# Kernel tuning notes

Hardware: AMD Instinct MI355X
Metric: run time of the kernel (lower is better)

Reference implementation:

```python
import jax, jax.numpy as jnp
import numpy as np
from functools import partial

LEAK = 1.0 / 3.0   # scn default leakiness 0.333
EPS = 1e-4         # scn BatchNormalization default eps


def linkey(c, S):
    return (c[..., 0] * S + c[..., 1]) * S + c[..., 2]


def sub_offsets(K):
    r = K // 2
    g = np.stack(np.meshgrid(*([np.arange(-r, r + 1)] * 3), indexing='ij'), -1).reshape(-1, 3)
    return jnp.asarray(g, jnp.int32)


def down_offsets(s):
    g = np.stack(np.meshgrid(*([np.arange(s)] * 3), indexing='ij'), -1).reshape(-1, 3)
    return jnp.asarray(g, jnp.int32)


@partial(jax.checkpoint, static_argnums=(4, 5))
def sparse_conv(out_coords, in_coords, in_feats, W, S_in, stride, offsets):
    """Rulebook gather-GEMM-scatter via sorted-key binary search.
    out_coords [M,3], in_coords [N,3] sorted by linearized key, in_feats [N,Cin],
    W [K3,Cin,Cout]. Submanifold: stride=1, centered offsets, out_coords==in_coords.
    Strided scn.Convolution: offsets 0..stride-1, out sites = unique(in//stride)."""
    in_keys = linkey(in_coords, S_in)  # sorted [N]
    Nin = in_keys.shape[0]

    def body(acc, kw):
        off, Wk = kw
        child = out_coords * stride + off                       # [M,3]
        valid = jnp.all((child >= 0) & (child < S_in), axis=-1)
        nkey = linkey(child, S_in)
        idx = jnp.searchsorted(in_keys, nkey)
        idxc = jnp.clip(idx, 0, Nin - 1)
        found = valid & (in_keys[idxc] == nkey)
        g = jnp.where(found[:, None], in_feats[idxc], 0.0)      # gather, zero for inactive
        return acc + g @ Wk, None

    acc0 = jnp.zeros((out_coords.shape[0], W.shape[-1]), in_feats.dtype)
    acc, _ = jax.lax.scan(body, acc0, (offsets, W))
    return acc


def bn_lrelu(x, g, b):
    m = x.mean(0)
    v = x.var(0)
    y = (x - m) * (g / jnp.sqrt(v + EPS)) + b
    return jnp.where(y > 0, y, LEAK * y)


def lrelu(x):
    return jnp.where(x > 0, x, LEAK * x)


def forward_core(floats, c0, c1, c2, c3, c4):
    (feats0, W_init, Wd1, gd1, bd1, W11a, g11, b11, W11b,
     W12a, g12, b12, W12b, Wd2, gd2, bd2,
     W21a, g21, b21, W21b, W22a, g22, b22, W22b,
     Wd3, gd3, bd3, Wd4, gd4, bd4, W2, b2, W3, b3) = floats
    o3 = sub_offsets(3)
    x = sparse_conv(c0, c0, feats0, W_init, 512, 1, sub_offsets(7))                 # [N0,64] @512
    x = bn_lrelu(sparse_conv(c1, c0, x, Wd1, 512, 2, down_offsets(2)), gd1, bd1)    # [N1,64] @256
    res = x
    h = bn_lrelu(sparse_conv(c1, c1, x, W11a, 256, 1, o3), g11, b11)
    x = lrelu(sparse_conv(c1, c1, h, W11b, 256, 1, o3) + res)
    res = x
    h = bn_lrelu(sparse_conv(c1, c1, x, W12a, 256, 1, o3), g12, b12)
    x = lrelu(sparse_conv(c1, c1, h, W12b, 256, 1, o3) + res)
    x = bn_lrelu(sparse_conv(c2, c1, x, Wd2, 256, 2, down_offsets(2)), gd2, bd2)    # [N2,128] @128
    res = x
    h = bn_lrelu(sparse_conv(c2, c2, x, W21a, 128, 1, o3), g21, b21)
    x = lrelu(sparse_conv(c2, c2, h, W21b, 128, 1, o3) + res)
    res = x
    h = bn_lrelu(sparse_conv(c2, c2, x, W22a, 128, 1, o3), g22, b22)
    x = lrelu(sparse_conv(c2, c2, h, W22b, 128, 1, o3) + res)
    x = bn_lrelu(sparse_conv(c3, c2, x, Wd3, 128, 4, down_offsets(4)), gd3, bd3)    # [N3,64] @32
    x = bn_lrelu(sparse_conv(c4, c3, x, Wd4, 32, 4, down_offsets(4)), gd4, bd4)     # [N4,2]  @8
    # SparseToDense -> dense [2,8,8,8], then torch .view(-1, 2*8*8*8) (channel-major)
    k4 = linkey(c4, 8)
    dense = jnp.zeros((8 * 8 * 8, 2), x.dtype).at[k4].set(x)    # [512,2]
    flat = dense.T.reshape(1, -1)                               # [1,1024]
    v = jax.nn.elu(flat @ W2 + b2)
    return jax.nn.sigmoid(v @ W3 + b3)                          # [1,1]


def _decode(k, S):
    a = k // (S * S)
    r = k % (S * S)
    return np.stack([a, r // S, r % S], -1).astype(np.int32)


def setup_inputs() -> dict:
    rng = np.random.default_rng(0)
    N0 = 50000
    k0 = np.unique(rng.integers(0, 512 ** 3, size=N0 + 20000))[:N0]
    c0 = _decode(k0, 512)
    c1 = _decode(np.unique((c0[:, 0].astype(np.int64) // 2 * 256 + c0[:, 1] // 2) * 256 + c0[:, 2] // 2), 256)
    c2 = _decode(np.unique((c1[:, 0].astype(np.int64) // 2 * 128 + c1[:, 1] // 2) * 128 + c1[:, 2] // 2), 128)
    c3 = _decode(np.unique((c2[:, 0].astype(np.int64) // 4 * 32 + c2[:, 1] // 4) * 32 + c2[:, 2] // 4), 32)
    c4 = _decode(np.unique((c3[:, 0].astype(np.int64) // 4 * 8 + c3[:, 1] // 4) * 8 + c3[:, 2] // 4), 8)
    key = jax.random.key(0)
    ks = jax.random.split(key, 20)

    def w(i, shape, fan):
        return jax.random.normal(ks[i], shape, jnp.float32) / np.float32(np.sqrt(fan))

    return dict(
        feats0=jax.random.normal(ks[0], (N0, 1), jnp.float32),
        W_init=w(1, (343, 1, 64), 343.0),
        Wd1=w(2, (8, 64, 64), 8 * 64), gd1=jnp.ones(64), bd1=jnp.zeros(64),
        W11a=w(3, (27, 64, 64), 27 * 64), g11=jnp.ones(64), b11=jnp.zeros(64),
        W11b=w(4, (27, 64, 64), 27 * 64),
        W12a=w(5, (27, 64, 64), 27 * 64), g12=jnp.ones(64), b12=jnp.zeros(64),
        W12b=w(6, (27, 64, 64), 27 * 64),
        Wd2=w(7, (8, 64, 128), 8 * 64), gd2=jnp.ones(128), bd2=jnp.zeros(128),
        W21a=w(8, (27, 128, 128), 27 * 128), g21=jnp.ones(128), b21=jnp.zeros(128),
        W21b=w(9, (27, 128, 128), 27 * 128),
        W22a=w(10, (27, 128, 128), 27 * 128), g22=jnp.ones(128), b22=jnp.zeros(128),
        W22b=w(11, (27, 128, 128), 27 * 128),
        Wd3=w(12, (64, 128, 64), 64 * 128), gd3=jnp.ones(64), bd3=jnp.zeros(64),
        Wd4=w(13, (64, 64, 2), 64 * 64), gd4=jnp.ones(2), bd4=jnp.zeros(2),
        W2=w(14, (1024, 2), 1024.0), b2=jnp.zeros(2),
        W3=w(15, (2, 1), 2.0), b3=jnp.zeros(1),
        coords0=jnp.asarray(c0), coords1=jnp.asarray(c1), coords2=jnp.asarray(c2),
        coords3=jnp.asarray(c3), coords4=jnp.asarray(c4),
    )


def reference(feats0, W_init, Wd1, gd1, bd1, W11a, g11, b11, W11b, W12a, g12, b12, W12b,
              Wd2, gd2, bd2, W21a, g21, b21, W21b, W22a, g22, b22, W22b,
              Wd3, gd3, bd3, Wd4, gd4, bd4, W2, b2, W3, b3,
              coords0, coords1, coords2, coords3, coords4):
    floats = (feats0, W_init, Wd1, gd1, bd1, W11a, g11, b11, W11b, W12a, g12, b12, W12b,
              Wd2, gd2, bd2, W21a, g21, b21, W21b, W22a, g22, b22, W22b,
              Wd3, gd3, bd3, Wd4, gd4, bd4, W2, b2, W3, b3)
    return forward_core(floats, coords0, coords1, coords2, coords3, coords4)
```

## Files before the change

### kernel.cpp

```cpp
#include <hip/hip_runtime.h>

#define LEAKF (1.0f/3.0f)
#define BN_EPS 1e-4f

__device__ __forceinline__ unsigned hmix(int key) {
    unsigned h = (unsigned)key * 2654435761u;
    h ^= h >> 15;
    return h;
}

__device__ __forceinline__ int hlookup(const int* __restrict__ hk,
                                       const int* __restrict__ hv,
                                       int mask, int key) {
    unsigned h = hmix(key) & (unsigned)mask;
    while (true) {
        int k = hk[h];
        if (k == key) return hv[h];
        if (k == -1) return -1;
        h = (h + 1) & (unsigned)mask;
    }
}

__device__ __forceinline__ float bnl(float v, float s, float h) {
    v = v * s + h;
    return v > 0.f ? v : v * LEAKF;
}

__global__ __launch_bounds__(256) void build_hash_bm_all(
    int B0, int B1, int B2,
    int N0, const int* __restrict__ c0, int* __restrict__ hk0, int* __restrict__ hv0,
    int m0, unsigned* __restrict__ bm0,
    int N1, const int* __restrict__ c1, int* __restrict__ hk1, int* __restrict__ hv1,
    int m1, unsigned* __restrict__ bm1,
    int N2, const int* __restrict__ c2, int* __restrict__ hk2, int* __restrict__ hv2,
    int m2, unsigned* __restrict__ bm2,
    int N3, const int* __restrict__ c3, int* __restrict__ hk3, int* __restrict__ hv3,
    int m3) {
    const int* coords; int* hk; int* hv; unsigned* bm; int mask, S, N, i;
    int b = blockIdx.x;
    if (b < B0)           { coords = c0; hk = hk0; hv = hv0; bm = bm0; mask = m0; S = 512; N = N0; i = b * 256 + threadIdx.x; }
    else if (b < B0 + B1) { coords = c1; hk = hk1; hv = hv1; bm = bm1; mask = m1; S = 256; N = N1; i = (b - B0) * 256 + threadIdx.x; }
    else if (b < B0 + B1 + B2) { coords = c2; hk = hk2; hv = hv2; bm = bm2; mask = m2; S = 128; N = N2; i = (b - B0 - B1) * 256 + threadIdx.x; }
    else                  { coords = c3; hk = hk3; hv = hv3; bm = nullptr; mask = m3; S = 32; N = N3; i = (b - B0 - B1 - B2) * 256 + threadIdx.x; }
    if (i >= N) return;
    int key = (coords[3 * i] * S + coords[3 * i + 1]) * S + coords[3 * i + 2];
    if (bm) atomicOr(&bm[key >> 5], 1u << (key & 31));
    unsigned h = hmix(key) & (unsigned)mask;
    while (true) {
        int old = atomicCAS(&hk[h], -1, key);
        if (old == -1 || old == key) { hv[h] = i; break; }
        h = (h + 1) & (unsigned)mask;
    }
}

__global__ __launch_bounds__(256) void rb_sub_bm(
    int B1,
    int N1, const int* __restrict__ c1, const unsigned* __restrict__ bm1,
    const int* __restrict__ hk1, const int* __restrict__ hv1, int m1,
    int2* __restrict__ rb1, int* __restrict__ cnt1, int cap1,
    int N2, const int* __restrict__ c2, const unsigned* __restrict__ bm2,
    const int* __restrict__ hk2, const int* __restrict__ hv2, int m2,
    int2* __restrict__ rb2, int* __restrict__ cnt2, int cap2) {
    __shared__ int lcnt[27];
    __shared__ int lbase[27];
    int tid = threadIdx.x;
    if (tid < 27) lcnt[tid] = 0;
    __syncthreads();
    const int* coords; const unsigned* bm; const int* hk; const int* hv;
    int mask, S, N, t; int2* pairs; int* counts; int cap;
    if (blockIdx.x < B1) {
        coords = c1; bm = bm1; hk = hk1; hv = hv1; mask = m1; S = 256; N = N1;
        pairs = rb1; counts = cnt1; cap = cap1; t = blockIdx.x * 256 + tid;
    } else {
        coords = c2; bm = bm2; hk = hk2; hv = hv2; mask = m2; S = 128; N = N2;
        pairs = rb2; counts = cnt2; cap = cap2; t = (blockIdx.x - B1) * 256 + tid;
    }
    unsigned bits = 0;
    int m = 0, kmin = 0, z = 0, dx = 0, dy = 0;
    int rk[3], ix[3];
    if (t < N * 9) {
        m = t / 9;
        int od = t - m * 9;
        dx = od / 3 - 1;
        dy = od - (od / 3) * 3 - 1;
        int x = coords[3 * m] + dx;
        int y = coords[3 * m + 1] + dy;
        z = coords[3 * m + 2];
        if ((unsigned)x < (unsigned)S && (unsigned)y < (unsigned)S) {
            int zmin = z - 1 < 0 ? 0 : z - 1;
            int zmax = z + 1 > S - 1 ? S - 1 : z + 1;
            kmin = (x * S + y) * S + zmin;
            int wi = kmin >> 5, sh = kmin & 31, nb = zmax - zmin + 1;
            unsigned long long w =
                ((unsigned long long)bm[wi + 1] << 32) | (unsigned long long)bm[wi];
            bits = (unsigned)((w >> sh) & ((1u << nb) - 1u));
            if (dx == 0 && dy == 0) bits &= ~(1u << (z - zmin));
            unsigned tmp = bits;
            int nf = 0;
            while (tmp) {
                int bb = __ffs(tmp) - 1;
                tmp &= tmp - 1;
                ix[nf] = hlookup(hk, hv, mask, kmin + bb);
                int dz = (kmin & (S - 1)) + bb - z;
                int k = (dx + 1) * 9 + (dy + 1) * 3 + (dz + 1);
                rk[nf] = atomicAdd(&lcnt[k], 1);
                nf++;
            }
        }
    }
    __syncthreads();
    if (tid < 27 && lcnt[tid] > 0) lbase[tid] = atomicAdd(&counts[tid], lcnt[tid]);
    __syncthreads();
    {
        unsigned tmp = bits;
        int j = 0;
        while (tmp) {
            int bb = __ffs(tmp) - 1;
            tmp &= tmp - 1;
            int dz = (kmin & (S - 1)) + bb - z;
            int k = (dx + 1) * 9 + (dy + 1) * 3 + (dz + 1);
            int p = lbase[k] + rk[j];
            if (p < cap) pairs[(size_t)k * cap + p] = make_int2(m, ix[j]);
            j++;
        }
    }
}

__global__ __launch_bounds__(256) void rb_down_all(
    int B1, int B2,
    int N0, const int* __restrict__ c0, const int* __restrict__ hk1,
    const int* __restrict__ hv1, int m1, int2* __restrict__ rbD1,
    int* __restrict__ cntD1, int capD1,
    int N1, const int* __restrict__ c1, const int* __restrict__ hk2,
    const int* __restrict__ hv2, int m2, int2* __restrict__ rbD2,
    int* __restrict__ cntD2, int capD2,
    int N2, const int* __restrict__ c2, const int* __restrict__ hk3,
    const int* __restrict__ hv3, int m3, int2* __restrict__ rbD3,
    int* __restrict__ cntD3, int capD3) {
    __shared__ int lcnt[64];
    __shared__ int lbase[64];
    int tid = threadIdx.x;
    const int* cin; const int* hk; const int* hv;
    int mask, Sout, s, Nin, i; int2* pairs; int* counts; int cap;
    int b = blockIdx.x;
    if (b < B1) {
        cin = c0; hk = hk1; hv = hv1; mask = m1; Sout = 256; s = 2; Nin = N0;
        pairs = rbD1; counts = cntD1; cap = capD1; i = b * 256 + tid;
    } else if (b < B1 + B2) {
        cin = c1; hk = hk2; hv = hv2; mask = m2; Sout = 128; s = 2; Nin = N1;
        pairs = rbD2; counts = cntD2; cap = capD2; i = (b - B1) * 256 + tid;
    } else {
        cin = c2; hk = hk3; hv = hv3; mask = m3; Sout = 32; s = 4; Nin = N2;
        pairs = rbD3; counts = cntD3; cap = capD3; i = (b - B1 - B2) * 256 + tid;
    }
    int K3 = s * s * s;
    if (tid < K3) lcnt[tid] = 0;
    __syncthreads();
    int k = -1, m = -1, rank = 0;
    if (i < Nin) {
        int x = cin[3 * i], y = cin[3 * i + 1], z = cin[3 * i + 2];
        k = ((x % s) * s + (y % s)) * s + (z % s);
        int key = ((x / s) * Sout + (y / s)) * Sout + (z / s);
        m = hlookup(hk, hv, mask, key);
        rank = atomicAdd(&lcnt[k], 1);
    }
    __syncthreads();
    if (tid < K3 && lcnt[tid] > 0) lbase[tid] = atomicAdd(&counts[tid], lcnt[tid]);
    __syncthreads();
    if (i < Nin) {
        int p = lbase[k] + rank;
        if (p < cap) pairs[(size_t)k * cap + p] = make_int2(m, i);
    }
}

__global__ __launch_bounds__(256) void init_probe(
    int total, int chunk, const int* __restrict__ c0, const unsigned* __restrict__ bm,
    const int* __restrict__ hk, const int* __restrict__ hv, int mask,
    int2* __restrict__ pairs, int* __restrict__ pcount, int cap) {
    __shared__ int lcnt, lbase;
    int tid = threadIdx.x;
    if (tid == 0) lcnt = 0;
    __syncthreads();
    int b = blockIdx.x;
    int nb = (b & 7) * chunk + (b >> 3);
    int t = nb * 256 + tid;
    unsigned bitsArr[7];
    int kminArr[7];
#pragma unroll
    for (int j = 0; j < 7; j++) { bitsArr[j] = 0; kminArr[j] = 0; }
    int m = -1, z = 0, dx = 0, rank = 0, found = 0;
    if (t < total) {
        m = t / 7;
        dx = t - m * 7 - 3;
        int x = c0[3 * m] + dx;
        int cy = c0[3 * m + 1];
        z = c0[3 * m + 2];
        if ((unsigned)x < 512u) {
            int zmin = z - 3 < 0 ? 0 : z - 3;
            int zmax = z + 3 > 511 ? 511 : z + 3;
            int nbits = zmax - zmin + 1;
#pragma unroll
            for (int j = 0; j < 7; j++) {
                int y = cy + j - 3;
                if ((unsigned)y < 512u) {
                    int kmin = (x * 512 + y) * 512 + zmin;
                    kminArr[j] = kmin;
                    int wi = kmin >> 5, sh = kmin & 31;
                    unsigned long long w =
                        ((unsigned long long)bm[wi + 1] << 32) | (unsigned long long)bm[wi];
                    unsigned bits = (unsigned)((w >> sh) & ((1u << nbits) - 1u));
                    if (dx == 0 && j == 3) bits &= ~(1u << (z - zmin));
                    bitsArr[j] = bits;
                    found += __popc(bits);
                }
            }
        }
    }
    if (found) rank = atomicAdd(&lcnt, found);
    __syncthreads();
    if (tid == 0 && lcnt > 0) lbase = atomicAdd(pcount, lcnt);
    __syncthreads();
    if (found) {
        int p = lbase + rank;
#pragma unroll
        for (int j = 0; j < 7; j++) {
            unsigned bits = bitsArr[j];
            while (bits) {
                int b2 = __ffs(bits) - 1;
                bits &= bits - 1;
                int nkey = kminArr[j] + b2;
                int idx = hlookup(hk, hv, mask, nkey);
                int dz = (kminArr[j] & 511) + b2 - z;
                int k = (dx + 3) * 49 + j * 7 + (dz + 3);
                if (p < cap) pairs[p] = make_int2(m, idx | (k << 17));
                p++;
            }
        }
    }
}

__global__ __launch_bounds__(256) void init_center(
    int N0, const float* __restrict__ f0, const float* __restrict__ W,
    float* __restrict__ out) {
    int t = blockIdx.x * 256 + threadIdx.x;
    if (t >= N0 * 64) return;
    int m = t >> 6, co = t & 63;
    out[t] = f0[m] * W[171 * 64 + co];
}

__global__ __launch_bounds__(256) void init_apply(
    const int2* __restrict__ pairs, const int* __restrict__ pcount, int cap,
    const float* __restrict__ f0, const float* __restrict__ W,
    float* __restrict__ out) {
    int P = min(*pcount, cap);
    int t = blockIdx.x * 256 + threadIdx.x;
    if (t >= P * 64) return;
    int p = t >> 6, co = t & 63;
    int2 pr = pairs[p];
    int idx = pr.y & 0x1FFFF, k = pr.y >> 17;
    atomicAdd(&out[(size_t)pr.x * 64 + co], f0[idx] * W[k * 64 + co]);
}

template <int C, int TS, bool BNF>
__global__ __launch_bounds__(256) void center_gemm(
    int N, const float* __restrict__ inF, const float* __restrict__ Wc,
    float* __restrict__ out, const float* __restrict__ scp,
    const float* __restrict__ shp) {
    constexpr int C4 = C / 4;
    constexpr int SP = TS / 8;
    __shared__ float sW[C * 64];
    __shared__ float4 sRow[TS * C4];
    int tid = threadIdx.x;
    int t0 = blockIdx.x * TS;
    int co0 = blockIdx.y << 6;
    for (int e = tid; e < C * 16; e += 256) {
        int ci = e >> 4, c4 = e & 15;
        ((float4*)sW)[e] = *(const float4*)(Wc + (size_t)ci * C + co0 + c4 * 4);
    }
    for (int e = tid; e < TS * C4; e += 256) {
        int p = e / C4, c4 = e - p * C4;
        float4 v = make_float4(0.f, 0.f, 0.f, 0.f);
        if (t0 + p < N) {
            v = ((const float4*)inF)[(size_t)(t0 + p) * C4 + c4];
            if (BNF) {
                float4 s4 = ((const float4*)scp)[c4];
                float4 h4 = ((const float4*)shp)[c4];
                v.x = bnl(v.x, s4.x, h4.x);
                v.y = bnl(v.y, s4.y, h4.y);
                v.z = bnl(v.z, s4.z, h4.z);
                v.w = bnl(v.w, s4.w, h4.w);
            }
        }
        sRow[e] = v;
    }
    __syncthreads();
    int co = tid & 31, sg = tid >> 5;
    float accA[SP], accB[SP];
#pragma unroll
    for (int j = 0; j < SP; j++) { accA[j] = 0.f; accB[j] = 0.f; }
    for (int c4 = 0; c4 < C4; c4++) {
        float a0 = sW[(c4 * 4 + 0) * 64 + co];
        float a1 = sW[(c4 * 4 + 1) * 64 + co];
        float a2 = sW[(c4 * 4 + 2) * 64 + co];
        float a3 = sW[(c4 * 4 + 3) * 64 + co];
        float b0 = sW[(c4 * 4 + 0) * 64 + co + 32];
        float b1 = sW[(c4 * 4 + 1) * 64 + co + 32];
        float b2 = sW[(c4 * 4 + 2) * 64 + co + 32];
        float b3 = sW[(c4 * 4 + 3) * 64 + co + 32];
#pragma unroll
        for (int j = 0; j < SP; j++) {
            float4 r = sRow[(sg * SP + j) * C4 + c4];
            accA[j] += r.x * a0 + r.y * a1 + r.z * a2 + r.w * a3;
            accB[j] += r.x * b0 + r.y * b1 + r.z * b2 + r.w * b3;
        }
    }
#pragma unroll
    for (int j = 0; j < SP; j++) {
        int p = sg * SP + j;
        if (t0 + p < N) {
            out[(size_t)(t0 + p) * C + co0 + co] = accA[j];
            out[(size_t)(t0 + p) * C + co0 + co + 32] = accB[j];
        }
    }
}

template <int CIN, int P, int MODE>
__global__ __launch_bounds__(256) void pair_gemm(
    const float* __restrict__ inF, const float* __restrict__ inF2,
    const float* __restrict__ W, float* __restrict__ out,
    const int2* __restrict__ pairs, const int* __restrict__ counts,
    int cap, int chunksPerK, int totalNb, int COUT, int nslab,
    const float* __restrict__ scp, const float* __restrict__ shp) {
    constexpr int C4 = CIN / 4;
    constexpr int SP = P / 8;
    __shared__ float sW[CIN * 64];
    __shared__ float4 sRow[P * C4];
    __shared__ int sM[P];
    __shared__ int sIdx[P];
    int b = blockIdx.x;
    int nb = (b & 7) * (gridDim.x >> 3) + (b >> 3);
    if (nb >= totalNb) return;
    int k = nb / chunksPerK;
    int chunk = nb - k * chunksPerK;
    int cnt = min(counts[k], cap);
    int base = chunk * P;
    if (base >= cnt) return;
    int Pact = min(P, cnt - base);
    int tid = threadIdx.x;
    if (tid < P) {
        if (tid < Pact) {
            int2 pr = pairs[(size_t)k * cap + base + tid];
            sM[tid] = pr.x;
            sIdx[tid] = pr.y;
        } else {
            sM[tid] = -1;
            sIdx[tid] = 0;
        }
    }
    __syncthreads();
    int co = tid & 31, sg = tid >> 5;
    for (int s = 0; s < nslab; s++) {
        int co0 = s << 6;
        if (s > 0) __syncthreads();
        const float* gW = W + (size_t)k * CIN * COUT + co0;
        for (int e = tid; e < CIN * 16; e += 256) {
            int ci = e >> 4, c4 = e & 15;
            ((float4*)sW)[e] = *(const float4*)(gW + (size_t)ci * COUT + c4 * 4);
        }
        if (s == 0) {
            for (int e = tid; e < P * C4; e += 256) {
                int p = e / C4, c4 = e - p * C4;
                float4 v = make_float4(0.f, 0.f, 0.f, 0.f);
                if (p < Pact) {
                    v = ((const float4*)inF)[(size_t)sIdx[p] * C4 + c4];
                    if (MODE == 1) {
                        float4 s4 = ((const float4*)scp)[c4];
                        float4 h4 = ((const float4*)shp)[c4];
                        v.x = bnl(v.x, s4.x, h4.x);
                        v.y = bnl(v.y, s4.y, h4.y);
                        v.z = bnl(v.z, s4.z, h4.z);
                        v.w = bnl(v.w, s4.w, h4.w);
                    } else if (MODE == 2) {
                        float4 u = ((const float4*)inF2)[(size_t)sIdx[p] * C4 + c4];
                        v.x += u.x; v.y += u.y; v.z += u.z; v.w += u.w;
                        v.x = v.x > 0.f ? v.x : v.x * LEAKF;
                        v.y = v.y > 0.f ? v.y : v.y * LEAKF;
                        v.z = v.z > 0.f ? v.z : v.z * LEAKF;
                        v.w = v.w > 0.f ? v.w : v.w * LEAKF;
                    }
                }
                sRow[e] = v;
            }
        }
        __syncthreads();
        float accA[SP], accB[SP];
#pragma unroll
        for (int j = 0; j < SP; j++) { accA[j] = 0.f; accB[j] = 0.f; }
        for (int c4 = 0; c4 < C4; c4++) {
            float a0 = sW[(c4 * 4 + 0) * 64 + co];
            float a1 = sW[(c4 * 4 + 1) * 64 + co];
            float a2 = sW[(c4 * 4 + 2) * 64 + co];
            float a3 = sW[(c4 * 4 + 3) * 64 + co];
            float b0 = sW[(c4 * 4 + 0) * 64 + co + 32];
            float b1 = sW[(c4 * 4 + 1) * 64 + co + 32];
            float b2 = sW[(c4 * 4 + 2) * 64 + co + 32];
            float b3 = sW[(c4 * 4 + 3) * 64 + co + 32];
#pragma unroll
            for (int j = 0; j < SP; j++) {
                float4 r = sRow[(sg * SP + j) * C4 + c4];
                accA[j] += r.x * a0 + r.y * a1 + r.z * a2 + r.w * a3;
                accB[j] += r.x * b0 + r.y * b1 + r.z * b2 + r.w * b3;
            }
        }
#pragma unroll
        for (int j = 0; j < SP; j++) {
            int p = sg * SP + j;
            if (p < Pact) {
                atomicAdd(&out[(size_t)sM[p] * COUT + co0 + co], accA[j]);
                atomicAdd(&out[(size_t)sM[p] * COUT + co0 + co + 32], accB[j]);
            }
        }
    }
}

__global__ __launch_bounds__(256) void bn_reduce_fin(
    const float4* __restrict__ X4, int total4, int B4, int C, int Cmask, float invN,
    const float* __restrict__ g, const float* __restrict__ b,
    float* __restrict__ sums, int* __restrict__ done,
    float* __restrict__ sc, float* __restrict__ sh) {
    __shared__ float sS[128];
    __shared__ float sQ[128];
    __shared__ int isLast;
    int tid = threadIdx.x;
    if (tid < C) { sS[tid] = 0.f; sQ[tid] = 0.f; }
    __syncthreads();
    int base4 = blockIdx.x * B4;
    int end4 = min(base4 + B4, total4);
    float s0 = 0.f, s1 = 0.f, s2 = 0.f, s3 = 0.f;
    float q0 = 0.f, q1 = 0.f, q2 = 0.f, q3 = 0.f;
    for (int e4 = base4 + tid; e4 < end4; e4 += 256) {
        float4 v = X4[e4];
        s0 += v.x; q0 += v.x * v.x;
        s1 += v.y; q1 += v.y * v.y;
        s2 += v.z; q2 += v.z * v.z;
        s3 += v.w; q3 += v.w * v.w;
    }
    int c0 = (4 * (base4 + tid)) & Cmask;
    atomicAdd(&sS[c0], s0);               atomicAdd(&sQ[c0], q0);
    atomicAdd(&sS[(c0 + 1) & Cmask], s1); atomicAdd(&sQ[(c0 + 1) & Cmask], q1);
    atomicAdd(&sS[(c0 + 2) & Cmask], s2); atomicAdd(&sQ[(c0 + 2) & Cmask], q2);
    atomicAdd(&sS[(c0 + 3) & Cmask], s3); atomicAdd(&sQ[(c0 + 3) & Cmask], q3);
    __syncthreads();
    if (tid < C) {
        atomicAdd(&sums[tid], sS[tid]);
        atomicAdd(&sums[128 + tid], sQ[tid]);
    }
    __syncthreads();
    if (tid == 0) {
        __threadfence();
        int t = atomicAdd(done, 1);
        isLast = (t == (int)gridDim.x - 1);
    }
    __syncthreads();
    if (isLast) {
        if (tid < C) {
            float v1 = atomicAdd(&sums[tid], 0.0f);
            float v2 = atomicAdd(&sums[128 + tid], 0.0f);
            float mean = v1 * invN;
            float var = v2 * invN - mean * mean;
            float s = g[tid] / sqrtf(var + BN_EPS);
            sc[tid] = s;
            sh[tid] = b[tid] - mean * s;
            sums[tid] = 0.f;
            sums[128 + tid] = 0.f;
        }
        if (tid == 0) *done = 0;
    }
}

__global__ __launch_bounds__(256) void add_lrelu_bn(const float4* __restrict__ A,
                                                    const float4* __restrict__ X,
                                                    float4* __restrict__ Y, int total4,
                                                    int C4mask,
                                                    const float* __restrict__ scp,
                                                    const float* __restrict__ shp) {
    int e = blockIdx.x * 256 + threadIdx.x;
    if (e >= total4) return;
    int c4 = e & C4mask;
    float4 s4 = ((const float4*)scp)[c4];
    float4 h4 = ((const float4*)shp)[c4];
    float4 a = A[e], x = X[e], v;
    v.x = a.x + bnl(x.x, s4.x, h4.x);
    v.y = a.y + bnl(x.y, s4.y, h4.y);
    v.z = a.z + bnl(x.z, s4.z, h4.z);
    v.w = a.w + bnl(x.w, s4.w, h4.w);
    v.x = v.x > 0.f ? v.x : v.x * LEAKF;
    v.y = v.y > 0.f ? v.y : v.y * LEAKF;
    v.z = v.z > 0.f ? v.z : v.z * LEAKF;
    v.w = v.w > 0.f ? v.w : v.w * LEAKF;
    Y[e] = v;
}

__global__ __launch_bounds__(64) void tail_kernel(
    int M, const int* __restrict__ oc, const float* __restrict__ x3,
    const float* __restrict__ W, float* __restrict__ x4,
    const int* __restrict__ hk, const int* __restrict__ hv, int mask,
    const float* __restrict__ scp, const float* __restrict__ shp,
    const float* __restrict__ g4, const float* __restrict__ b4,
    const float* __restrict__ W2, const float* __restrict__ b2,
    const float* __restrict__ W3, const float* __restrict__ b3,
    int* __restrict__ ticket, float* __restrict__ out) {
    __shared__ int sIdx[64];
    __shared__ int sK[64];
    __shared__ int sCount;
    __shared__ int isLast;
    __shared__ float sDense[1024];
    __shared__ float sS[2], sQ[2], ssc[2], ssh[2];
    int m = blockIdx.x, tid = threadIdx.x;
    int cx = oc[3 * m], cy = oc[3 * m + 1], cz = oc[3 * m + 2];
    if (tid == 0) sCount = 0;
    __syncthreads();
    {
        int k = tid;
        int a = k >> 4, b = (k >> 2) & 3, c = k & 3;
        int x = cx * 4 + a, y = cy * 4 + b, z = cz * 4 + c;
        int key = (x * 32 + y) * 32 + z;
        int idx = hlookup(hk, hv, mask, key);
        if (idx >= 0) { int p = atomicAdd(&sCount, 1); sIdx[p] = idx; sK[p] = k; }
    }
    __syncthreads();
    int cnt = sCount;
    float s = scp[tid], h = shp[tid];
    float a0 = 0.f, a1 = 0.f;
    for (int j = 0; j < cnt; j++) {
        int idx = sIdx[j], k = sK[j];
        float f = bnl(x3[(size_t)idx * 64 + tid], s, h);
        const float* wk = W + ((size_t)k * 64 + tid) * 2;
        a0 += f * wk[0];
        a1 += f * wk[1];
    }
    for (int o = 32; o > 0; o >>= 1) {
        a0 += __shfl_down(a0, o);
        a1 += __shfl_down(a1, o);
    }
    if (tid == 0) { x4[2 * m] = a0; x4[2 * m + 1] = a1; }
    __threadfence();
    if (tid == 0) {
        int t = atomicAdd(ticket, 1);
        isLast = (t == (int)gridDim.x - 1);
    }
    __syncthreads();
    if (!isLast) return;
    if (tid < 2) { sS[tid] = 0.f; sQ[tid] = 0.f; }
    for (int i = tid; i < 1024; i += 64) sDense[i] = 0.f;
    __syncthreads();
    float ls = 0.f, lq = 0.f;
    for (int i = tid; i < 2 * M; i += 64) {
        float v = atomicAdd(&x4[i], 0.0f);
        ls += v; lq += v * v;
    }
    atomicAdd(&sS[tid & 1], ls);
    atomicAdd(&sQ[tid & 1], lq);
    __syncthreads();
    if (tid < 2) {
        float mean = sS[tid] / (float)M;
        float var = sQ[tid] / (float)M - mean * mean;
        float sc = g4[tid] / sqrtf(var + BN_EPS);
        ssc[tid] = sc;
        ssh[tid] = b4[tid] - mean * sc;
    }
    __syncthreads();
    for (int i = tid; i < 2 * M; i += 64) {
        int mm = i >> 1, co = i & 1;
        float v = atomicAdd(&x4[i], 0.0f) * ssc[co] + ssh[co];
        v = v > 0.f ? v : v * LEAKF;
        int key = (oc[3 * mm] * 8 + oc[3 * mm + 1]) * 8 + oc[3 * mm + 2];
        sDense[key * 2 + co] = v;
    }
    __syncthreads();
    float h0 = 0.f, h1 = 0.f;
    for (int j = tid; j < 1024; j += 64) {
        int co = j >> 9, k = j & 511;
        float f = sDense[k * 2 + co];
        h0 += f * W2[2 * j];
        h1 += f * W2[2 * j + 1];
    }
    for (int o = 32; o > 0; o >>= 1) {
        h0 += __shfl_down(h0, o);
        h1 += __shfl_down(h1, o);
    }
    if (tid == 0) {
        float v0 = h0 + b2[0];
        float v1 = h1 + b2[1];
        v0 = v0 > 0.f ? v0 : expm1f(v0);
        v1 = v1 > 0.f ? v1 : expm1f(v1);
        float z = v0 * W3[0] + v1 * W3[1] + b3[0];
        out[0] = 1.f / (1.f + expf(-z));
    }
}

extern "C" void kernel_launch(void* const* d_in, const int* in_sizes, int n_in,
                              void* d_out, int out_size, void* d_ws, size_t ws_size,
                              hipStream_t stream) {
    const float* F0    = (const float*)d_in[0];
    const float* Winit = (const float*)d_in[1];
    const float* Wd1   = (const float*)d_in[2];
    const float* gd1   = (const float*)d_in[3];
    const float* bd1   = (const float*)d_in[4];
    const float* W11a  = (const float*)d_in[5];
    const float* g11   = (const float*)d_in[6];
    const float* b11   = (const float*)d_in[7];
    const float* W11b  = (const float*)d_in[8];
    const float* W12a  = (const float*)d_in[9];
    const float* g12   = (const float*)d_in[10];
    const float* b12   = (const float*)d_in[11];
    const float* W12b  = (const float*)d_in[12];
    const float* Wd2   = (const float*)d_in[13];
    const float* gd2   = (const float*)d_in[14];
    const float* bd2   = (const float*)d_in[15];
    const float* W21a  = (const float*)d_in[16];
    const float* g21   = (const float*)d_in[17];
    const float* b21   = (const float*)d_in[18];
    const float* W21b  = (const float*)d_in[19];
    const float* W22a  = (const float*)d_in[20];
    const float* g22   = (const float*)d_in[21];
    const float* b22   = (const float*)d_in[22];
    const float* W22b  = (const float*)d_in[23];
    const float* Wd3   = (const float*)d_in[24];
    const float* gd3   = (const float*)d_in[25];
    const float* bd3   = (const float*)d_in[26];
    const float* Wd4   = (const float*)d_in[27];
    const float* gd4   = (const float*)d_in[28];
    const float* bd4   = (const float*)d_in[29];
    const float* W2    = (const float*)d_in[30];
    const float* b2    = (const float*)d_in[31];
    const float* W3    = (const float*)d_in[32];
    const float* b3    = (const float*)d_in[33];
    const int* c0 = (const int*)d_in[34];
    const int* c1 = (const int*)d_in[35];
    const int* c2 = (const int*)d_in[36];
    const int* c3 = (const int*)d_in[37];
    const int* c4 = (const int*)d_in[38];
    int N0 = in_sizes[34] / 3, N1 = in_sizes[35] / 3, N2 = in_sizes[36] / 3;
    int N3 = in_sizes[37] / 3, N4 = in_sizes[38] / 3;

    char* base = (char*)d_ws;
    size_t off = 0;
    auto alloc = [&](size_t bytes) -> void* {
        void* p = base + off;
        off = (off + bytes + 255) & ~(size_t)255;
        return p;
    };
    const int CAP0 = 262144, CAP = 131072, CAP3 = 65536;
    size_t hs_off = off;
    int* hk0 = (int*)alloc((size_t)CAP0 * 4);
    int* hv0 = (int*)alloc((size_t)CAP0 * 4);
    int* hk1 = (int*)alloc((size_t)CAP * 4);
    int* hv1 = (int*)alloc((size_t)CAP * 4);
    int* hk2 = (int*)alloc((size_t)CAP * 4);
    int* hv2 = (int*)alloc((size_t)CAP * 4);
    int* hk3 = (int*)alloc((size_t)CAP3 * 4);
    int* hv3 = (int*)alloc((size_t)CAP3 * 4);
    size_t he_off = off;
    size_t zs_off = off;
    float* sums = (float*)alloc(256 * 4);
    float* scb = (float*)alloc(8 * 128 * 4);
    float* shb = (float*)alloc(8 * 128 * 4);
    float* x4 = (float*)alloc(1032 * 4);
    int* counts = (int*)alloc(136 * 4);
    unsigned* bm1 = (unsigned*)alloc((size_t)(524288 + 2) * 4);
    unsigned* bm2 = (unsigned*)alloc((size_t)(65536 + 2) * 4);
    size_t ze_off = off;
    int* cntS1 = counts, *cntS2 = counts + 27, *cntD1 = counts + 54, *cntD2 = counts + 62,
       * cntD3 = counts + 70;
    int* done = counts + 134;
    int* pcount = counts + 135;
    const int CAP_S1 = 1024, CAP_S2 = 4096, CAP_D1 = 8192, CAP_D2 = 8192, CAP_D3 = 1024;
    const int CAPP = 16384;
    int2* pairs0 = (int2*)alloc((size_t)CAPP * 8);
    int2* rbS1 = (int2*)alloc((size_t)27 * CAP_S1 * 8);
    int2* rbS2 = (int2*)alloc((size_t)27 * CAP_S2 * 8);
    int2* rbD1 = (int2*)alloc((size_t)8 * CAP_D1 * 8);
    int2* rbD2 = (int2*)alloc((size_t)8 * CAP_D2 * 8);
    int2* rbD3 = (int2*)alloc((size_t)64 * CAP_D3 * 8);
    size_t relems = (size_t)N0 * 64;
    if ((size_t)N2 * 128 > relems) relems = (size_t)N2 * 128;
    float* R1 = (float*)alloc(relems * 4);
    float* R2 = (float*)alloc(relems * 4);
    float* R3 = (float*)alloc(relems * 4);
    unsigned* bm0 = (unsigned*)R1;

    hipMemsetAsync(base + hs_off, 0xFF, he_off - hs_off, stream);
    hipMemsetAsync(base + zs_off, 0x00, ze_off - zs_off, stream);
    hipMemsetAsync(bm0, 0x00, (size_t)(1 << 24) + 64, stream);

    int Bh0 = (N0 + 255) / 256, Bh1 = (N1 + 255) / 256, Bh2 = (N2 + 255) / 256,
        Bh3 = (N3 + 255) / 256;
    build_hash_bm_all<<<Bh0 + Bh1 + Bh2 + Bh3, 256, 0, stream>>>(
        Bh0, Bh1, Bh2,
        N0, c0, hk0, hv0, CAP0 - 1, bm0,
        N1, c1, hk1, hv1, CAP - 1, bm1,
        N2, c2, hk2, hv2, CAP - 1, bm2,
        N3, c3, hk3, hv3, CAP3 - 1);
    int Bs1 = (N1 * 9 + 255) / 256, Bs2 = (N2 * 9 + 255) / 256;
    rb_sub_bm<<<Bs1 + Bs2, 256, 0, stream>>>(
        Bs1,
        N1, c1, bm1, hk1, hv1, CAP - 1, rbS1, cntS1, CAP_S1,
        N2, c2, bm2, hk2, hv2, CAP - 1, rbS2, cntS2, CAP_S2);
    rb_down_all<<<Bh0 + Bh1 + Bh2, 256, 0, stream>>>(
        Bh0, Bh1,
        N0, c0, hk1, hv1, CAP - 1, rbD1, cntD1, CAP_D1,
        N1, c1, hk2, hv2, CAP - 1, rbD2, cntD2, CAP_D2,
        N2, c2, hk3, hv3, CAP3 - 1, rbD3, cntD3, CAP_D3);

    auto bnstats = [&](const float* X, int N, int C, const float* g, const float* b,
                       int slot) {
        int total4 = (N * C + 3) >> 2;
        int B4 = 32 * C;
        int grid = (total4 + B4 - 1) / B4;
        bn_reduce_fin<<<grid, 256, 0, stream>>>((const float4*)X, total4, B4, C, C - 1,
                                                1.0f / (float)N, g, b, sums, done,
                                                scb + slot * 128, shb + slot * 128);
    };
    const int CH_S1 = CAP_S1 / 64;
    const int CH_S2 = CAP_S2 / 32;
    const int CH_D12 = CAP_D1 / 64;
    const int CH_D3 = CAP_D3 / 32;
    auto sub64 = [&](const float* X, const float* W, float* Y, int slot) {
        if (slot >= 0) {
            center_gemm<64, 64, true><<<dim3((N1 + 63) / 64, 1), 256, 0, stream>>>(
                N1, X, W + 13 * 64 * 64, Y, scb + slot * 128, shb + slot * 128);
            pair_gemm<64, 64, 1><<<27 * CH_S1, 256, 0, stream>>>(
                X, nullptr, W, Y, rbS1, cntS1, CAP_S1, CH_S1, 27 * CH_S1, 64, 1,
                scb + slot * 128, shb + slot * 128);
        } else {
            center_gemm<64, 64, false><<<dim3((N1 + 63) / 64, 1), 256, 0, stream>>>(
                N1, X, W + 13 * 64 * 64, Y, nullptr, nullptr);
            pair_gemm<64, 64, 0><<<27 * CH_S1, 256, 0, stream>>>(
                X, nullptr, W, Y, rbS1, cntS1, CAP_S1, CH_S1, 27 * CH_S1, 64, 1,
                nullptr, nullptr);
        }
    };
    auto sub128 = [&](const float* X, const float* W, float* Y, int slot) {
        if (slot >= 0) {
            center_gemm<128, 48, true><<<dim3((N2 + 47) / 48, 2), 256, 0, stream>>>(
                N2, X, W + 13 * 128 * 128, Y, scb + slot * 128, shb + slot * 128);
            pair_gemm<128, 32, 1><<<27 * CH_S2, 256, 0, stream>>>(
                X, nullptr, W, Y, rbS2, cntS2, CAP_S2, CH_S2, 27 * CH_S2, 128, 2,
                scb + slot * 128, shb + slot * 128);
        } else {
            center_gemm<128, 48, false><<<dim3((N2 + 47) / 48, 2), 256, 0, stream>>>(
                N2, X, W + 13 * 128 * 128, Y, nullptr, nullptr);
            pair_gemm<128, 32, 0><<<27 * CH_S2, 256, 0, stream>>>(
                X, nullptr, W, Y, rbS2, cntS2, CAP_S2, CH_S2, 27 * CH_S2, 128, 2,
                nullptr, nullptr);
        }
    };

    int totProbe = N0 * 7;
    int Gp = (totProbe + 255) / 256;
    int chunkP = (Gp + 7) / 8;
    init_probe<<<8 * chunkP, 256, 0, stream>>>(totProbe, chunkP, c0, bm0,
                                               hk0, hv0, CAP0 - 1, pairs0, pcount, CAPP);
    init_center<<<(N0 * 64 + 255) / 256, 256, 0, stream>>>(N0, F0, Winit, R3);
    init_apply<<<(CAPP * 64) / 256, 256, 0, stream>>>(pairs0, pcount, CAPP, F0, Winit, R3);

    hipMemsetAsync(R1, 0, (size_t)N1 * 64 * 4, stream);
    pair_gemm<64, 64, 0><<<8 * CH_D12, 256, 0, stream>>>(
        R3, nullptr, Wd1, R1, rbD1, cntD1, CAP_D1, CH_D12, 8 * CH_D12, 64, 1,
        nullptr, nullptr);
    bnstats(R1, N1, 64, gd1, bd1, 0);

    sub64(R1, W11a, R2, 0);
    bnstats(R2, N1, 64, g11, b11, 1);
    sub64(R2, W11b, R3, 1);
    add_lrelu_bn<<<(N1 * 16 + 255) / 256, 256, 0, stream>>>(
        (const float4*)R3, (const float4*)R1, (float4*)R2, N1 * 16, 15, scb, shb);
    sub64(R2, W12a, R3, -1);
    bnstats(R3, N1, 64, g12, b12, 2);
    sub64(R3, W12b, R1, 2);

    hipMemsetAsync(R3, 0, (size_t)N2 * 128 * 4, stream);
    pair_gemm<64, 64, 2><<<8 * CH_D12, 256, 0, stream>>>(
        R1, R2, Wd2, R3, rbD2, cntD2, CAP_D2, CH_D12, 8 * CH_D12, 128, 2,
        nullptr, nullptr);
    bnstats(R3, N2, 128, gd2, bd2, 3);

    sub128(R3, W21a, R1, 3);
    bnstats(R1, N2, 128, g21, b21, 4);
    sub128(R1, W21b, R2, 4);
    add_lrelu_bn<<<(N2 * 32 + 255) / 256, 256, 0, stream>>>(
        (const float4*)R2, (const float4*)R3, (float4*)R1, N2 * 32, 31,
        scb + 3 * 128, shb + 3 * 128);
    sub128(R1, W22a, R2, -1);
    bnstats(R2, N2, 128, g22, b22, 5);
    sub128(R2, W22b, R3, 5);

    hipMemsetAsync(R2, 0, (size_t)N3 * 64 * 4, stream);
    pair_gemm<128, 32, 2><<<64 * CH_D3, 256, 0, stream>>>(
        R3, R1, Wd3, R2, rbD3, cntD3, CAP_D3, CH_D3, 64 * CH_D3, 64, 1,
        nullptr, nullptr);
    bnstats(R2, N3, 64, gd3, bd3, 6);

    tail_kernel<<<N4, 64, 0, stream>>>(N4, c4, R2, Wd4, x4, hk3, hv3, CAP3 - 1,
                                       scb + 6 * 128, shb + 6 * 128, gd4, bd4,
                                       W2, b2, W3, b3, done, (float*)d_out);
}
```

Baseline: 1.095 ms.

## Replace stride-2 downsample rulebooks with output-stationary gather-GEMM kernel

Drops the rulebook build and atomic-scatter pair_gemm for the first two stride-2 downsampling convolutions. Each block now owns 32 output sites, finds their 8 children with bitmap plus hash lookups, and accumulates in shared memory before one plain store, so the memsets and scatter atomics go away. The residual add and leaky ReLU are fused into the gather for the second downsample. Buffer roles are reshuffled to match. The cost is one block-wide sync per offset and weights reloaded into shared memory per block.

```diff
diff --git a/kernel.cpp b/kernel.cpp
--- a/kernel.cpp
+++ b/kernel.cpp
@@ -126,50 +126,124 @@
     }
 }
 
-__global__ __launch_bounds__(256) void rb_down_all(
-    int B1, int B2,
-    int N0, const int* __restrict__ c0, const int* __restrict__ hk1,
-    const int* __restrict__ hv1, int m1, int2* __restrict__ rbD1,
-    int* __restrict__ cntD1, int capD1,
-    int N1, const int* __restrict__ c1, const int* __restrict__ hk2,
-    const int* __restrict__ hv2, int m2, int2* __restrict__ rbD2,
-    int* __restrict__ cntD2, int capD2,
-    int N2, const int* __restrict__ c2, const int* __restrict__ hk3,
-    const int* __restrict__ hv3, int m3, int2* __restrict__ rbD3,
-    int* __restrict__ cntD3, int capD3) {
+__global__ __launch_bounds__(256) void rb_down3(
+    int Nin, const int* __restrict__ cin,
+    const int* __restrict__ hk, const int* __restrict__ hv, int mask,
+    int2* __restrict__ pairs, int* __restrict__ counts, int cap) {
     __shared__ int lcnt[64];
     __shared__ int lbase[64];
     int tid = threadIdx.x;
-    const int* cin; const int* hk; const int* hv;
-    int mask, Sout, s, Nin, i; int2* pairs; int* counts; int cap;
-    int b = blockIdx.x;
-    if (b < B1) {
-        cin = c0; hk = hk1; hv = hv1; mask = m1; Sout = 256; s = 2; Nin = N0;
-        pairs = rbD1; counts = cntD1; cap = capD1; i = b * 256 + tid;
-    } else if (b < B1 + B2) {
-        cin = c1; hk = hk2; hv = hv2; mask = m2; Sout = 128; s = 2; Nin = N1;
-        pairs = rbD2; counts = cntD2; cap = capD2; i = (b - B1) * 256 + tid;
-    } else {
-        cin = c2; hk = hk3; hv = hv3; mask = m3; Sout = 32; s = 4; Nin = N2;
-        pairs = rbD3; counts = cntD3; cap = capD3; i = (b - B1 - B2) * 256 + tid;
-    }
-    int K3 = s * s * s;
-    if (tid < K3) lcnt[tid] = 0;
-    __syncthreads();
+    if (tid < 64) lcnt[tid] = 0;
+    __syncthreads();
+    int i = blockIdx.x * 256 + tid;
     int k = -1, m = -1, rank = 0;
     if (i < Nin) {
         int x = cin[3 * i], y = cin[3 * i + 1], z = cin[3 * i + 2];
-        k = ((x % s) * s + (y % s)) * s + (z % s);
-        int key = ((x / s) * Sout + (y / s)) * Sout + (z / s);
+        k = ((x % 4) * 4 + (y % 4)) * 4 + (z % 4);
+        int key = ((x / 4) * 32 + (y / 4)) * 32 + (z / 4);
         m = hlookup(hk, hv, mask, key);
         rank = atomicAdd(&lcnt[k], 1);
     }
     __syncthreads();
-    if (tid < K3 && lcnt[tid] > 0) lbase[tid] = atomicAdd(&counts[tid], lcnt[tid]);
+    if (tid < 64 && lcnt[tid] > 0) lbase[tid] = atomicAdd(&counts[tid], lcnt[tid]);
     __syncthreads();
     if (i < Nin) {
         int p = lbase[k] + rank;
         if (p < cap) pairs[(size_t)k * cap + p] = make_int2(m, i);
+    }
+}
+
+template <int CIN, int COUT, int MODE>
+__global__ __launch_bounds__(256) void down_os2(
+    int Nout, int G, int chunk, int Sout, const int* __restrict__ oc,
+    const float* __restrict__ inF, const float* __restrict__ inF2,
+    const unsigned* __restrict__ bm, const int* __restrict__ hk,
+    const int* __restrict__ hv, int mask,
+    const float* __restrict__ W, float* __restrict__ out) {
+    constexpr int T = 32;
+    constexpr int C4 = CIN / 4;
+    constexpr int NCO = COUT / 32;
+    __shared__ float sAcc[T * COUT];
+    __shared__ float sW[CIN * COUT];
+    __shared__ float4 sRow[T * C4];
+    __shared__ int entJ[8 * T];
+    __shared__ int entI[8 * T];
+    __shared__ int nk[8];
+    int b = blockIdx.x;
+    int nb = (b & 7) * chunk + (b >> 3);
+    if (nb >= G) return;
+    int tid = threadIdx.x;
+    if (tid < 8) nk[tid] = 0;
+    for (int e = tid; e < T * COUT / 4; e += 256)
+        ((float4*)sAcc)[e] = make_float4(0.f, 0.f, 0.f, 0.f);
+    __syncthreads();
+    int m0 = nb * T;
+    {
+        int j = tid >> 3, k = tid & 7;
+        int m = m0 + j;
+        if (m < Nout) {
+            int Sin = Sout * 2;
+            int x = oc[3 * m] * 2 + (k >> 2);
+            int y = oc[3 * m + 1] * 2 + ((k >> 1) & 1);
+            int z = oc[3 * m + 2] * 2 + (k & 1);
+            int key = (x * Sin + y) * Sin + z;
+            if ((bm[key >> 5] >> (key & 31)) & 1u) {
+                int idx = hlookup(hk, hv, mask, key);
+                int p = atomicAdd(&nk[k], 1);
+                entJ[k * T + p] = j;
+                entI[k * T + p] = idx;
+            }
+        }
+    }
+    __syncthreads();
+    int co = tid & 31, eg = tid >> 5;
+    for (int k = 0; k < 8; k++) {
+        int n = nk[k];
+        if (n == 0) continue;
+        __syncthreads();
+        const float* gW = W + (size_t)k * CIN * COUT;
+        for (int e = tid; e < CIN * COUT / 4; e += 256)
+            ((float4*)sW)[e] = ((const float4*)gW)[e];
+        for (int e = tid; e < n * C4; e += 256) {
+            int p = e / C4, c4 = e - p * C4;
+            float4 v = ((const float4*)inF)[(size_t)entI[k * T + p] * C4 + c4];
+            if (MODE == 2) {
+                float4 u = ((const float4*)inF2)[(size_t)entI[k * T + p] * C4 + c4];
+                v.x += u.x; v.y += u.y; v.z += u.z; v.w += u.w;
+                v.x = v.x > 0.f ? v.x : v.x * LEAKF;
+                v.y = v.y > 0.f ? v.y : v.y * LEAKF;
+                v.z = v.z > 0.f ? v.z : v.z * LEAKF;
+                v.w = v.w > 0.f ? v.w : v.w * LEAKF;
+            }
+            sRow[p * C4 + c4] = v;
+        }
+        __syncthreads();
+        for (int e = eg; e < n; e += 8) {
+            int j = entJ[k * T + e];
+            float acc[NCO];
+#pragma unroll
+            for (int q = 0; q < NCO; q++) acc[q] = 0.f;
+            for (int c4 = 0; c4 < C4; c4++) {
+                float4 r = sRow[e * C4 + c4];
+#pragma unroll
+                for (int q = 0; q < NCO; q++) {
+                    int c = co + q * 32;
+                    acc[q] += r.x * sW[(c4 * 4 + 0) * COUT + c] +
+                              r.y * sW[(c4 * 4 + 1) * COUT + c] +
+                              r.z * sW[(c4 * 4 + 2) * COUT + c] +
+                              r.w * sW[(c4 * 4 + 3) * COUT + c];
+                }
+            }
+#pragma unroll
+            for (int q = 0; q < NCO; q++) sAcc[j * COUT + co + q * 32] += acc[q];
+        }
+    }
+    __syncthreads();
+    for (int e = tid; e < T * COUT / 4; e += 256) {
+        int j = e / (COUT / 4);
+        if (m0 + j < Nout)
+            ((float4*)(out + (size_t)(m0 + j) * COUT))[e - j * (COUT / 4)] =
+                ((float4*)sAcc)[e];
     }
 }
 
@@ -671,17 +745,14 @@
     unsigned* bm1 = (unsigned*)alloc((size_t)(524288 + 2) * 4);
     unsigned* bm2 = (unsigned*)alloc((size_t)(65536 + 2) * 4);
     size_t ze_off = off;
-    int* cntS1 = counts, *cntS2 = counts + 27, *cntD1 = counts + 54, *cntD2 = counts + 62,
-       * cntD3 = counts + 70;
+    int* cntS1 = counts, *cntS2 = counts + 27, *cntD3 = counts + 70;
     int* done = counts + 134;
     int* pcount = counts + 135;
-    const int CAP_S1 = 1024, CAP_S2 = 4096, CAP_D1 = 8192, CAP_D2 = 8192, CAP_D3 = 1024;
+    const int CAP_S1 = 1024, CAP_S2 = 4096, CAP_D3 = 1024;
     const int CAPP = 16384;
     int2* pairs0 = (int2*)alloc((size_t)CAPP * 8);
     int2* rbS1 = (int2*)alloc((size_t)27 * CAP_S1 * 8);
     int2* rbS2 = (int2*)alloc((size_t)27 * CAP_S2 * 8);
-    int2* rbD1 = (int2*)alloc((size_t)8 * CAP_D1 * 8);
-    int2* rbD2 = (int2*)alloc((size_t)8 * CAP_D2 * 8);
     int2* rbD3 = (int2*)alloc((size_t)64 * CAP_D3 * 8);
     size_t relems = (size_t)N0 * 64;
     if ((size_t)N2 * 128 > relems) relems = (size_t)N2 * 128;
@@ -707,11 +778,7 @@
         Bs1,
         N1, c1, bm1, hk1, hv1, CAP - 1, rbS1, cntS1, CAP_S1,
         N2, c2, bm2, hk2, hv2, CAP - 1, rbS2, cntS2, CAP_S2);
-    rb_down_all<<<Bh0 + Bh1 + Bh2, 256, 0, stream>>>(
-        Bh0, Bh1,
-        N0, c0, hk1, hv1, CAP - 1, rbD1, cntD1, CAP_D1,
-        N1, c1, hk2, hv2, CAP - 1, rbD2, cntD2, CAP_D2,
-        N2, c2, hk3, hv3, CAP3 - 1, rbD3, cntD3, CAP_D3);
+    rb_down3<<<Bh2, 256, 0, stream>>>(N2, c2, hk3, hv3, CAP3 - 1, rbD3, cntD3, CAP_D3);
 
     auto bnstats = [&](const float* X, int N, int C, const float* g, const float* b,
                        int slot) {
@@ -724,7 +791,6 @@
     };
     const int CH_S1 = CAP_S1 / 64;
     const int CH_S2 = CAP_S2 / 32;
-    const int CH_D12 = CAP_D1 / 64;
     const int CH_D3 = CAP_D3 / 32;
     auto sub64 = [&](const float* X, const float* W, float* Y, int slot) {
         if (slot >= 0) {
@@ -765,32 +831,34 @@
     init_center<<<(N0 * 64 + 255) / 256, 256, 0, stream>>>(N0, F0, Winit, R3);
     init_apply<<<(CAPP * 64) / 256, 256, 0, stream>>>(pairs0, pcount, CAPP, F0, Winit, R3);
 
-    hipMemsetAsync(R1, 0, (size_t)N1 * 64 * 4, stream);
-    pair_gemm<64, 64, 0><<<8 * CH_D12, 256, 0, stream>>>(
-        R3, nullptr, Wd1, R1, rbD1, cntD1, CAP_D1, CH_D12, 8 * CH_D12, 64, 1,
-        nullptr, nullptr);
-    bnstats(R1, N1, 64, gd1, bd1, 0);
-
-    sub64(R1, W11a, R2, 0);
-    bnstats(R2, N1, 64, g11, b11, 1);
-    sub64(R2, W11b, R3, 1);
+    {
+        int G = (N1 + 31) / 32, ch = (G + 7) / 8;
+        down_os2<64, 64, 0><<<8 * ch, 256, 0, stream>>>(
+            N1, G, ch, 256, c1, R3, nullptr, bm0, hk0, hv0, CAP0 - 1, Wd1, R2);
+    }
+    bnstats(R2, N1, 64, gd1, bd1, 0);
+
+    sub64(R2, W11a, R1, 0);
+    bnstats(R1, N1, 64, g11, b11, 1);
+    sub64(R1, W11b, R3, 1);
     add_lrelu_bn<<<(N1 * 16 + 255) / 256, 256, 0, stream>>>(
-        (const float4*)R3, (const float4*)R1, (float4*)R2, N1 * 16, 15, scb, shb);
-    sub64(R2, W12a, R3, -1);
-    bnstats(R3, N1, 64, g12, b12, 2);
-    sub64(R3, W12b, R1, 2);
-
-    hipMemsetAsync(R3, 0, (size_t)N2 * 128 * 4, stream);
-    pair_gemm<64, 64, 2><<<8 * CH_D12, 256, 0, stream>>>(
-        R1, R2, Wd2, R3, rbD2, cntD2, CAP_D2, CH_D12, 8 * CH_D12, 128, 2,
-        nullptr, nullptr);
-    bnstats(R3, N2, 128, gd2, bd2, 3);
-
-    sub128(R3, W21a, R1, 3);
+        (const float4*)R3, (const float4*)R2, (float4*)R1, N1 * 16, 15, scb, shb);
+    sub64(R1, W12a, R2, -1);
+    bnstats(R2, N1, 64, g12, b12, 2);
+    sub64(R2, W12b, R3, 2);
+
+    {
+        int G = (N2 + 31) / 32, ch = (G + 7) / 8;
+        down_os2<64, 128, 2><<<8 * ch, 256, 0, stream>>>(
+            N2, G, ch, 128, c2, R3, R1, bm1, hk1, hv1, CAP - 1, Wd2, R2);
+    }
+    bnstats(R2, N2, 128, gd2, bd2, 3);
+
+    sub128(R2, W21a, R1, 3);
     bnstats(R1, N2, 128, g21, b21, 4);
-    sub128(R1, W21b, R2, 4);
+    sub128(R1, W21b, R3, 4);
     add_lrelu_bn<<<(N2 * 32 + 255) / 256, 256, 0, stream>>>(
-        (const float4*)R2, (const float4*)R3, (float4*)R1, N2 * 32, 31,
+        (const float4*)R3, (const float4*)R2, (float4*)R1, N2 * 32, 31,
         scb + 3 * 128, shb + 3 * 128);
     sub128(R1, W22a, R2, -1);
     bnstats(R2, N2, 128, g22, b22, 5);
```

Measured after the change: 1.261 ms. +15.1%, slower.
